# Kernel optimization log

Hardware: AMD Instinct MI355X
Metric: run time of the kernel (lower is better)

Reference implementation:

```python
import jax, jax.numpy as jnp
import numpy as np


def setup_inputs() -> dict:
    key = jax.random.key(0)
    k1, k2 = jax.random.split(key)
    B, N, M, D = 32, 1024, 1024, 256
    h1 = jax.random.normal(k1, (B, N, D), dtype=jnp.float32)
    h2 = jax.random.normal(k2, (B, M, D), dtype=jnp.float32)
    return {"h1": h1, "h2": h2}


def reference(h1, h2):
    # Soft Hausdorff over B graph pairs.
    # torch cdist with p=2 here is sum_d |x-y|^2 == squared L2 distance;
    N = h1.shape[1]
    M = h2.shape[1]
    sq1 = jnp.sum(h1 * h1, axis=-1)  # [B, N]
    sq2 = jnp.sum(h2 * h2, axis=-1)  # [B, M]
    cross = jnp.einsum('bnd,bmd->bnm', h1, h2)  # [B, N, M]
    dist = sq1[:, :, None] + sq2[:, None, :] - 2.0 * cross
    dist = jnp.maximum(dist, 0.0)  # guard tiny negative fp noise
    a = jnp.min(dist, axis=1).sum(axis=-1)  # min over N for each col, then sum over M
    b = jnp.min(dist, axis=2).sum(axis=-1)  # min over M for each row, then sum over N
    return (a + b) / min(N, M)  # [B]
```

## Files before the change

kernel.cpp:

```cpp
#include <hip/hip_runtime.h>
#include <hip/hip_bf16.h>
#include <stdint.h>

#define BB 32
#define NN 1024
#define MM 1024
#define DD 256

typedef __attribute__((ext_vector_type(8))) short short8;
typedef __attribute__((ext_vector_type(4))) float floatx4;

__device__ inline unsigned short f2bf(float x) {
    union { __hip_bfloat16 h; unsigned short u; } cv;
    cv.h = __float2bfloat16(x);
    return cv.u;
}

__device__ inline void async_copy16(void* lds, const void* g) {
    __builtin_amdgcn_global_load_lds(
        (const __attribute__((address_space(1))) unsigned int*)g,
        (__attribute__((address_space(3))) unsigned int*)lds, 16, 0, 0);
}
__device__ inline void async_copy4(void* lds, const void* g) {
    __builtin_amdgcn_global_load_lds(
        (const __attribute__((address_space(1))) unsigned int*)g,
        (__attribute__((address_space(3))) unsigned int*)lds, 4, 0, 0);
}

__global__ __launch_bounds__(256) void convert_kernel(
        const float* __restrict__ h1, const float* __restrict__ h2,
        unsigned short* __restrict__ h1b, unsigned short* __restrict__ h2b,
        float* __restrict__ sq1, float* __restrict__ sq2,
        unsigned int* __restrict__ minb) {
    int g = blockIdx.x * 256 + threadIdx.x;
    if (g < 2 * BB * NN) minb[g] = 0x7F800000u;

    int wid  = blockIdx.x * 4 + (threadIdx.x >> 6);
    int lane = threadIdx.x & 63;
    int l5   = lane & 31;
    int row  = wid * 2 + (lane >> 5);
    const int total1 = BB * NN;

    const float* src; unsigned short* dst; float* sq; int r;
    if (row < total1) { src = h1; dst = h1b; sq = sq1; r = row; }
    else              { src = h2; dst = h2b; sq = sq2; r = row - total1; }

    const float4* p = (const float4*)(src + (size_t)r * DD) + l5 * 2;
    float4 a = p[0], c = p[1];

    float s = a.x*a.x + a.y*a.y + a.z*a.z + a.w*a.w
            + c.x*c.x + c.y*c.y + c.z*c.z + c.w*c.w;
    #pragma unroll
    for (int off = 16; off; off >>= 1) s += __shfl_xor(s, off, 64);

    short8 o;
    o[0] = f2bf(a.x); o[1] = f2bf(a.y); o[2] = f2bf(a.z); o[3] = f2bf(a.w);
    o[4] = f2bf(c.x); o[5] = f2bf(c.y); o[6] = f2bf(c.z); o[7] = f2bf(c.w);
    *(short8*)((char*)(dst + (size_t)r * DD) + l5 * 16) = o;

    if (l5 == 0) sq[r] = s;
}

__global__ __launch_bounds__(512, 2) void gemm_kernel(
        const unsigned short* __restrict__ h1b, const unsigned short* __restrict__ h2b,
        const float* __restrict__ sq1, const float* __restrict__ sq2,
        unsigned int* __restrict__ rowmin, unsigned int* __restrict__ colmin) {
    __shared__ __align__(16) char pool[106496];
    #define BUF0 (pool + 65536)
    #define BUF1 (pool + 81920)
    #define BUF2 (pool + 0)
    #define BUF3 (pool + 16384)
    float*        sq2_lds = (float*)(pool + 98304);
    unsigned int* cl      = (unsigned int*)(pool + 102400);

    const int b    = blockIdx.x;
    const int tile = blockIdx.y;
    const int n0   = tile * 128;

    const int tid  = threadIdx.x;
    const int wave = tid >> 6;
    const int lane = tid & 63;
    const int wn   = (wave >> 2) * 64;
    const int wm   = (wave & 3) * 32;

    const char* Ag = (const char*)(h1b + ((size_t)b * NN + n0) * DD);
    const char* Bg = (const char*)(h2b + (size_t)b * MM * DD);

    const int krow = lane >> 4;
    const int rrow = lane & 15;
    const int rx   = rrow & 7;
    const int lrow = krow * 4;
    const int lcol = rrow;

    cl[tid] = 0x7F800000u; cl[tid + 512] = 0x7F800000u;

    const float4* s1p = (const float4*)(sq1 + b * NN + n0 + wn + lrow);
    float4 s1v4[4];
    #pragma unroll
    for (int i = 0; i < 4; ++i) s1v4[i] = s1p[i * 4];

    #pragma unroll
    for (int t = 0; t < 2; ++t)
        async_copy4(pool + 98304 + t * 2048 + wave * 256,
                    (const char*)(sq2 + b * MM) + t * 2048 + wave * 256 + lane * 4);

    #pragma unroll
    for (int t = 0; t < 8; ++t) {
        int ch = t * 8 + wave;
        int r  = ch * 2 + (lane >> 5);
        int cu = (lane & 31) ^ (r & 7);
        async_copy16(pool + ch * 1024, Ag + (size_t)r * 512 + (cu << 4));
    }

    const int rl  = lane >> 3;
    const int bcu = (lane & 7) ^ rl;
    #define STAGE(mt_, ks_, BUFP)                                             \
        {                                                                     \
            _Pragma("unroll")                                                 \
            for (int c = 0; c < 2; ++c) {                                     \
                int ch_ = wave * 2 + c;                                       \
                int r_  = ch_ * 8 + rl;                                       \
                async_copy16((char*)(BUFP) + ch_ * 1024,                      \
                             Bg + (size_t)((mt_) * 128 + r_) * 512            \
                                + (size_t)(ks_) * 128 + (bcu << 4));          \
            }                                                                 \
        }

    STAGE(0, 0, BUF0);
    STAGE(0, 1, BUF1);

    asm volatile("s_waitcnt vmcnt(4)" ::: "memory");
    __builtin_amdgcn_s_barrier();
    __builtin_amdgcn_sched_barrier(0);

    short8 af[4][8];
    #pragma unroll
    for (int i = 0; i < 4; ++i) {
        #pragma unroll
        for (int kq = 0; kq < 8; ++kq) {
            int u = (kq * 4 + krow) ^ rx;
            af[i][kq] = *(const short8*)(pool
                        + (size_t)(wn + i * 16 + rrow) * 512 + (u << 4));
        }
    }
    asm volatile("s_waitcnt lgkmcnt(0)" ::: "memory");
    __builtin_amdgcn_s_barrier();
    __builtin_amdgcn_sched_barrier(0);
    STAGE(0, 2, BUF2);

    float rmin[4][4];
    #pragma unroll
    for (int i = 0; i < 4; ++i)
        #pragma unroll
        for (int r = 0; r < 4; ++r) rmin[i][r] = 3.0e38f;

    #pragma unroll 1
    for (int mt = 0; mt < 8; ++mt) {
        floatx4 acc[4][2] = {};

        #pragma unroll
        for (int ks = 0; ks < 4; ++ks) {
            if (mt == 7 && ks == 2)      { asm volatile("s_waitcnt vmcnt(2)" ::: "memory"); }
            else if (mt == 7 && ks == 3) { asm volatile("s_waitcnt vmcnt(0)" ::: "memory"); }
            else                         { asm volatile("s_waitcnt vmcnt(4)" ::: "memory"); }
            __builtin_amdgcn_s_barrier();
            __builtin_amdgcn_sched_barrier(0);

            if (ks == 0)          { STAGE(mt,     3, BUF3); }
            else if (mt < 7) {
                if (ks == 1)      { STAGE(mt + 1, 0, BUF0); }
                else if (ks == 2) { STAGE(mt + 1, 1, BUF1); }
                else              { STAGE(mt + 1, 2, BUF2); }
            }

            const char* Bb = (ks == 0) ? BUF0 : (ks == 1) ? BUF1
                           : (ks == 2) ? BUF2 : BUF3;
            __builtin_amdgcn_s_setprio(1);
            #pragma unroll
            for (int kk = 0; kk < 2; ++kk) {
                const int u = ((kk << 2) | krow) ^ rx;
                short8 bfv[2];
                #pragma unroll
                for (int j = 0; j < 2; ++j)
                    bfv[j] = *(const short8*)(Bb
                             + (size_t)(wm + j * 16 + rrow) * 128 + (u << 4));
                #pragma unroll
                for (int i = 0; i < 4; ++i)
                    #pragma unroll
                    for (int j = 0; j < 2; ++j)
                        acc[i][j] = __builtin_amdgcn_mfma_f32_16x16x32_bf16(
                            af[i][ks * 2 + kk], bfv[j], acc[i][j], 0, 0, 0);
            }
            __builtin_amdgcn_s_setprio(0);
        }

        float s2v0 = sq2_lds[mt * 128 + wm + lcol];
        float s2v1 = sq2_lds[mt * 128 + wm + 16 + lcol];

        float cmin0 = 3.0e38f, cmin1 = 3.0e38f;
        #pragma unroll
        for (int i = 0; i < 4; ++i) {
            #pragma unroll
            for (int r = 0; r < 4; ++r) {
                float s1x = ((const float*)&s1v4[i])[r];
                float d0 = fmaxf(s1x + s2v0 - 2.0f * acc[i][0][r], 0.0f);
                float d1 = fmaxf(s1x + s2v1 - 2.0f * acc[i][1][r], 0.0f);
                rmin[i][r] = fminf(rmin[i][r], fminf(d0, d1));
                cmin0 = fminf(cmin0, d0);
                cmin1 = fminf(cmin1, d1);
            }
        }
        cmin0 = fminf(cmin0, __shfl_xor(cmin0, 16, 64));
        cmin0 = fminf(cmin0, __shfl_xor(cmin0, 32, 64));
        cmin1 = fminf(cmin1, __shfl_xor(cmin1, 16, 64));
        cmin1 = fminf(cmin1, __shfl_xor(cmin1, 32, 64));
        if (lane < 16) {
            atomicMin(&cl[mt * 128 + wm + lcol],      __float_as_uint(cmin0));
            atomicMin(&cl[mt * 128 + wm + 16 + lcol], __float_as_uint(cmin1));
        }
    }

    unsigned int* rm = rowmin + b * NN + n0;
    #pragma unroll
    for (int i = 0; i < 4; ++i) {
        #pragma unroll
        for (int r = 0; r < 4; ++r) {
            float v = rmin[i][r];
            #pragma unroll
            for (int off = 1; off < 16; off <<= 1)
                v = fminf(v, __shfl_xor(v, off, 64));
            if (lcol == 0)
                atomicMin(&rm[wn + i * 16 + lrow + r], __float_as_uint(v));
        }
    }

    __syncthreads();
    unsigned int* cmg = colmin + b * MM;
    atomicMin(&cmg[tid],       cl[tid]);
    atomicMin(&cmg[tid + 512], cl[tid + 512]);
    #undef STAGE
    #undef BUF0
    #undef BUF1
    #undef BUF2
    #undef BUF3
}

__global__ __launch_bounds__(256) void finalize_kernel(
        const unsigned int* __restrict__ rowmin,
        const unsigned int* __restrict__ colmin,
        float* __restrict__ out) {
    int b = blockIdx.x;
    int tid = threadIdx.x;
    float s = 0.0f;
    for (int i = tid; i < NN; i += 256) s += __uint_as_float(rowmin[b * NN + i]);
    for (int i = tid; i < MM; i += 256) s += __uint_as_float(colmin[b * MM + i]);
    #pragma unroll
    for (int off = 32; off; off >>= 1) s += __shfl_xor(s, off, 64);
    __shared__ float wsum[4];
    if ((tid & 63) == 0) wsum[tid >> 6] = s;
    __syncthreads();
    if (tid == 0) out[b] = (wsum[0] + wsum[1] + wsum[2] + wsum[3]) * (1.0f / 1024.0f);
}

extern "C" void kernel_launch(void* const* d_in, const int* in_sizes, int n_in,
                              void* d_out, int out_size, void* d_ws, size_t ws_size,
                              hipStream_t stream) {
    const float* h1 = (const float*)d_in[0];
    const float* h2 = (const float*)d_in[1];
    float* out = (float*)d_out;

    char* ws = (char*)d_ws;
    const size_t bf_bytes = (size_t)BB * NN * DD * sizeof(unsigned short);
    unsigned short* h1b = (unsigned short*)ws;
    unsigned short* h2b = (unsigned short*)(ws + bf_bytes);
    float* sq1 = (float*)(ws + 2 * bf_bytes);
    float* sq2 = sq1 + BB * NN;
    unsigned int* rowmin = (unsigned int*)(sq2 + BB * MM);
    unsigned int* colmin = rowmin + BB * NN;

    hipLaunchKernelGGL(convert_kernel, dim3(8192), dim3(256), 0, stream,
                       h1, h2, h1b, h2b, sq1, sq2, rowmin);

    hipLaunchKernelGGL(gemm_kernel, dim3(BB, 8), dim3(512), 0, stream,
                       h1b, h2b, sq1, sq2, rowmin, colmin);

    hipLaunchKernelGGL(finalize_kernel, dim3(BB), dim3(256), 0, stream,
                       rowmin, colmin, out);
}
```

Measured before the change: 47.42 us.

## Fuse fp32-to-bf16 conversion and norms into GEMM, drop convert kernel

Removes the separate conversion kernel. The GEMM kernel now stages fp32 tiles of h1 and h2 directly into LDS, converts them to bf16 in registers before the MFMAs, and computes the squared norms on the fly. This avoids writing and re-reading a bf16 copy of both inputs and saves a kernel launch. In exchange, B tiles are twice as large in LDS (about 136KB, limiting residency to one block per CU), and every block repeats the conversion and norm VALU work for h2. Global atomics are replaced by per-tile column partials and direct row-min stores, with the min over tiles moved into the finalize kernel.

```diff
diff --git a/kernel.cpp b/kernel.cpp
--- a/kernel.cpp
+++ b/kernel.cpp
@@ -15,63 +15,25 @@
     cv.h = __float2bfloat16(x);
     return cv.u;
 }
-
+__device__ inline short8 pack8(float4 a, float4 b) {
+    short8 o;
+    o[0] = f2bf(a.x); o[1] = f2bf(a.y); o[2] = f2bf(a.z); o[3] = f2bf(a.w);
+    o[4] = f2bf(b.x); o[5] = f2bf(b.y); o[6] = f2bf(b.z); o[7] = f2bf(b.w);
+    return o;
+}
 __device__ inline void async_copy16(void* lds, const void* g) {
     __builtin_amdgcn_global_load_lds(
         (const __attribute__((address_space(1))) unsigned int*)g,
         (__attribute__((address_space(3))) unsigned int*)lds, 16, 0, 0);
 }
-__device__ inline void async_copy4(void* lds, const void* g) {
-    __builtin_amdgcn_global_load_lds(
-        (const __attribute__((address_space(1))) unsigned int*)g,
-        (__attribute__((address_space(3))) unsigned int*)lds, 4, 0, 0);
-}
-
-__global__ __launch_bounds__(256) void convert_kernel(
+
+__global__ __launch_bounds__(512, 2) void gemm_kernel(
         const float* __restrict__ h1, const float* __restrict__ h2,
-        unsigned short* __restrict__ h1b, unsigned short* __restrict__ h2b,
-        float* __restrict__ sq1, float* __restrict__ sq2,
-        unsigned int* __restrict__ minb) {
-    int g = blockIdx.x * 256 + threadIdx.x;
-    if (g < 2 * BB * NN) minb[g] = 0x7F800000u;
-
-    int wid  = blockIdx.x * 4 + (threadIdx.x >> 6);
-    int lane = threadIdx.x & 63;
-    int l5   = lane & 31;
-    int row  = wid * 2 + (lane >> 5);
-    const int total1 = BB * NN;
-
-    const float* src; unsigned short* dst; float* sq; int r;
-    if (row < total1) { src = h1; dst = h1b; sq = sq1; r = row; }
-    else              { src = h2; dst = h2b; sq = sq2; r = row - total1; }
-
-    const float4* p = (const float4*)(src + (size_t)r * DD) + l5 * 2;
-    float4 a = p[0], c = p[1];
-
-    float s = a.x*a.x + a.y*a.y + a.z*a.z + a.w*a.w
-            + c.x*c.x + c.y*c.y + c.z*c.z + c.w*c.w;
-    #pragma unroll
-    for (int off = 16; off; off >>= 1) s += __shfl_xor(s, off, 64);
-
-    short8 o;
-    o[0] = f2bf(a.x); o[1] = f2bf(a.y); o[2] = f2bf(a.z); o[3] = f2bf(a.w);
-    o[4] = f2bf(c.x); o[5] = f2bf(c.y); o[6] = f2bf(c.z); o[7] = f2bf(c.w);
-    *(short8*)((char*)(dst + (size_t)r * DD) + l5 * 16) = o;
-
-    if (l5 == 0) sq[r] = s;
-}
-
-__global__ __launch_bounds__(512, 2) void gemm_kernel(
-        const unsigned short* __restrict__ h1b, const unsigned short* __restrict__ h2b,
-        const float* __restrict__ sq1, const float* __restrict__ sq2,
-        unsigned int* __restrict__ rowmin, unsigned int* __restrict__ colmin) {
-    __shared__ __align__(16) char pool[106496];
-    #define BUF0 (pool + 65536)
-    #define BUF1 (pool + 81920)
-    #define BUF2 (pool + 0)
-    #define BUF3 (pool + 16384)
-    float*        sq2_lds = (float*)(pool + 98304);
-    unsigned int* cl      = (unsigned int*)(pool + 102400);
+        unsigned int* __restrict__ rowmin, unsigned int* __restrict__ colpart) {
+    __shared__ __align__(16) char pool[136192];
+    float*        sq1_lds = (float*)(pool + 131072);
+    unsigned int* cl      = (unsigned int*)(pool + 131584);
+    unsigned int* rlds    = (unsigned int*)(pool + 135680);
 
     const int b    = blockIdx.x;
     const int tile = blockIdx.y;
@@ -83,76 +45,79 @@
     const int wn   = (wave >> 2) * 64;
     const int wm   = (wave & 3) * 32;
 
-    const char* Ag = (const char*)(h1b + ((size_t)b * NN + n0) * DD);
-    const char* Bg = (const char*)(h2b + (size_t)b * MM * DD);
-
     const int krow = lane >> 4;
     const int rrow = lane & 15;
     const int rx   = rrow & 7;
     const int lrow = krow * 4;
     const int lcol = rrow;
 
+    const char* Ag = (const char*)(h1 + ((size_t)b * NN + n0) * DD);
+    const char* Bg = (const char*)(h2 + (size_t)b * MM * DD);
+
     cl[tid] = 0x7F800000u; cl[tid + 512] = 0x7F800000u;
-
-    const float4* s1p = (const float4*)(sq1 + b * NN + n0 + wn + lrow);
-    float4 s1v4[4];
-    #pragma unroll
-    for (int i = 0; i < 4; ++i) s1v4[i] = s1p[i * 4];
-
-    #pragma unroll
-    for (int t = 0; t < 2; ++t)
-        async_copy4(pool + 98304 + t * 2048 + wave * 256,
-                    (const char*)(sq2 + b * MM) + t * 2048 + wave * 256 + lane * 4);
-
-    #pragma unroll
-    for (int t = 0; t < 8; ++t) {
-        int ch = t * 8 + wave;
-        int r  = ch * 2 + (lane >> 5);
-        int cu = (lane & 31) ^ (r & 7);
-        async_copy16(pool + ch * 1024, Ag + (size_t)r * 512 + (cu << 4));
-    }
-
-    const int rl  = lane >> 3;
-    const int bcu = (lane & 7) ^ rl;
-    #define STAGE(mt_, ks_, BUFP)                                             \
-        {                                                                     \
-            _Pragma("unroll")                                                 \
-            for (int c = 0; c < 2; ++c) {                                     \
-                int ch_ = wave * 2 + c;                                       \
-                int r_  = ch_ * 8 + rl;                                       \
-                async_copy16((char*)(BUFP) + ch_ * 1024,                      \
-                             Bg + (size_t)((mt_) * 128 + r_) * 512            \
-                                + (size_t)(ks_) * 128 + (bcu << 4));          \
-            }                                                                 \
-        }
-
-    STAGE(0, 0, BUF0);
-    STAGE(0, 1, BUF1);
-
-    asm volatile("s_waitcnt vmcnt(4)" ::: "memory");
+    if (tid < 128) rlds[tid] = 0x7F800000u;
+
+    #pragma unroll
+    for (int t = 0; t < 16; ++t) {
+        int r = t * 8 + wave;
+        async_copy16(pool + r * 1024,
+                     Ag + (size_t)r * 1024 + ((lane ^ ((r & 7) << 1)) << 4));
+    }
+    asm volatile("s_waitcnt vmcnt(0) lgkmcnt(0)" ::: "memory");
     __builtin_amdgcn_s_barrier();
     __builtin_amdgcn_sched_barrier(0);
 
     short8 af[4][8];
-    #pragma unroll
-    for (int i = 0; i < 4; ++i) {
-        #pragma unroll
-        for (int kq = 0; kq < 8; ++kq) {
-            int u = (kq * 4 + krow) ^ rx;
-            af[i][kq] = *(const short8*)(pool
-                        + (size_t)(wn + i * 16 + rrow) * 512 + (u << 4));
+    {
+        float ssum[4] = {0.f, 0.f, 0.f, 0.f};
+        #pragma unroll
+        for (int i = 0; i < 4; ++i) {
+            const char* rp = pool + (size_t)(wn + i * 16 + rrow) * 1024;
+            #pragma unroll
+            for (int kq = 0; kq < 8; ++kq) {
+                int u0 = ((kq << 3) + (krow << 1)) ^ (rx << 1);
+                float4 f0 = *(const float4*)(rp + (u0 << 4));
+                float4 f1 = *(const float4*)(rp + ((u0 | 1) << 4));
+                af[i][kq] = pack8(f0, f1);
+                if ((wave & 3) == 0)
+                    ssum[i] += f0.x*f0.x + f0.y*f0.y + f0.z*f0.z + f0.w*f0.w
+                             + f1.x*f1.x + f1.y*f1.y + f1.z*f1.z + f1.w*f1.w;
+            }
+        }
+        if ((wave & 3) == 0) {
+            #pragma unroll
+            for (int i = 0; i < 4; ++i) {
+                float s = ssum[i];
+                s += __shfl_xor(s, 16, 64);
+                s += __shfl_xor(s, 32, 64);
+                if (lane < 16) sq1_lds[wn + i * 16 + rrow] = s;
+            }
         }
     }
     asm volatile("s_waitcnt lgkmcnt(0)" ::: "memory");
+    __builtin_amdgcn_sched_barrier(0);
     __builtin_amdgcn_s_barrier();
     __builtin_amdgcn_sched_barrier(0);
-    STAGE(0, 2, BUF2);
+
+    const int rl4 = lane >> 4;
+    const int pu  = lane & 15;
+    #define STAGE(mt_, ks_, boff_)                                            \
+        { _Pragma("unroll")                                                   \
+          for (int c = 0; c < 4; ++c) {                                       \
+            int ch_ = wave * 4 + c;                                           \
+            int r_  = ch_ * 4 + rl4;                                          \
+            async_copy16(pool + (boff_) + ch_ * 1024,                         \
+                Bg + (size_t)((mt_) * 128 + r_) * 1024 + (size_t)(ks_) * 256  \
+                   + ((pu ^ ((r_ & 7) << 1)) << 4)); } }
+
+    STAGE(0, 0, 0); STAGE(0, 1, 32768); STAGE(0, 2, 65536);
 
     float rmin[4][4];
     #pragma unroll
     for (int i = 0; i < 4; ++i)
         #pragma unroll
         for (int r = 0; r < 4; ++r) rmin[i][r] = 3.0e38f;
+    float s2a0 = 0.f, s2a1 = 0.f;
 
     #pragma unroll 1
     for (int mt = 0; mt < 8; ++mt) {
@@ -160,51 +125,57 @@
 
         #pragma unroll
         for (int ks = 0; ks < 4; ++ks) {
-            if (mt == 7 && ks == 2)      { asm volatile("s_waitcnt vmcnt(2)" ::: "memory"); }
+            if (mt == 7 && ks == 2)      { asm volatile("s_waitcnt vmcnt(4)" ::: "memory"); }
             else if (mt == 7 && ks == 3) { asm volatile("s_waitcnt vmcnt(0)" ::: "memory"); }
-            else                         { asm volatile("s_waitcnt vmcnt(4)" ::: "memory"); }
+            else                         { asm volatile("s_waitcnt vmcnt(8)" ::: "memory"); }
             __builtin_amdgcn_s_barrier();
             __builtin_amdgcn_sched_barrier(0);
 
-            if (ks == 0)          { STAGE(mt,     3, BUF3); }
+            if (ks == 0)          { STAGE(mt,     3, 98304); }
             else if (mt < 7) {
-                if (ks == 1)      { STAGE(mt + 1, 0, BUF0); }
-                else if (ks == 2) { STAGE(mt + 1, 1, BUF1); }
-                else              { STAGE(mt + 1, 2, BUF2); }
-            }
-
-            const char* Bb = (ks == 0) ? BUF0 : (ks == 1) ? BUF1
-                           : (ks == 2) ? BUF2 : BUF3;
+                if (ks == 1)      { STAGE(mt + 1, 0, 0);     }
+                else if (ks == 2) { STAGE(mt + 1, 1, 32768); }
+                else              { STAGE(mt + 1, 2, 65536); }
+            }
+
+            const char* Bb = pool + ((ks == 0) ? 0 : (ks == 1) ? 32768
+                                   : (ks == 2) ? 65536 : 98304);
             __builtin_amdgcn_s_setprio(1);
             #pragma unroll
             for (int kk = 0; kk < 2; ++kk) {
-                const int u = ((kk << 2) | krow) ^ rx;
-                short8 bfv[2];
                 #pragma unroll
-                for (int j = 0; j < 2; ++j)
-                    bfv[j] = *(const short8*)(Bb
-                             + (size_t)(wm + j * 16 + rrow) * 128 + (u << 4));
-                #pragma unroll
-                for (int i = 0; i < 4; ++i)
+                for (int j = 0; j < 2; ++j) {
+                    const char* rp = Bb + (size_t)(wm + j * 16 + rrow) * 256;
+                    int v0 = (((kk << 2) + krow) << 1) ^ (rx << 1);
+                    float4 g0 = *(const float4*)(rp + (v0 << 4));
+                    float4 g1 = *(const float4*)(rp + ((v0 | 1) << 4));
+                    short8 bv = pack8(g0, g1);
                     #pragma unroll
-                    for (int j = 0; j < 2; ++j)
+                    for (int i = 0; i < 4; ++i)
                         acc[i][j] = __builtin_amdgcn_mfma_f32_16x16x32_bf16(
-                            af[i][ks * 2 + kk], bfv[j], acc[i][j], 0, 0, 0);
+                            af[i][ks * 2 + kk], bv, acc[i][j], 0, 0, 0);
+                    float d = g0.x*g0.x + g0.y*g0.y + g0.z*g0.z + g0.w*g0.w
+                            + g1.x*g1.x + g1.y*g1.y + g1.z*g1.z + g1.w*g1.w;
+                    if (j == 0) s2a0 += d; else s2a1 += d;
+                }
             }
             __builtin_amdgcn_s_setprio(0);
         }
 
-        float s2v0 = sq2_lds[mt * 128 + wm + lcol];
-        float s2v1 = sq2_lds[mt * 128 + wm + 16 + lcol];
+        float s20 = s2a0; s20 += __shfl_xor(s20, 16, 64); s20 += __shfl_xor(s20, 32, 64);
+        float s21 = s2a1; s21 += __shfl_xor(s21, 16, 64); s21 += __shfl_xor(s21, 32, 64);
+        s2a0 = 0.f; s2a1 = 0.f;
 
         float cmin0 = 3.0e38f, cmin1 = 3.0e38f;
         #pragma unroll
         for (int i = 0; i < 4; ++i) {
+            float4 s1q = *(const float4*)((const char*)sq1_lds
+                        + ((wn + i * 16 + lrow) << 2));
             #pragma unroll
             for (int r = 0; r < 4; ++r) {
-                float s1x = ((const float*)&s1v4[i])[r];
-                float d0 = fmaxf(s1x + s2v0 - 2.0f * acc[i][0][r], 0.0f);
-                float d1 = fmaxf(s1x + s2v1 - 2.0f * acc[i][1][r], 0.0f);
+                float s1x = ((const float*)&s1q)[r];
+                float d0 = fmaxf(s1x + s20 - 2.0f * acc[i][0][r], 0.0f);
+                float d1 = fmaxf(s1x + s21 - 2.0f * acc[i][1][r], 0.0f);
                 rmin[i][r] = fminf(rmin[i][r], fminf(d0, d1));
                 cmin0 = fminf(cmin0, d0);
                 cmin1 = fminf(cmin1, d1);
@@ -220,7 +191,6 @@
         }
     }
 
-    unsigned int* rm = rowmin + b * NN + n0;
     #pragma unroll
     for (int i = 0; i < 4; ++i) {
         #pragma unroll
@@ -230,30 +200,35 @@
             for (int off = 1; off < 16; off <<= 1)
                 v = fminf(v, __shfl_xor(v, off, 64));
             if (lcol == 0)
-                atomicMin(&rm[wn + i * 16 + lrow + r], __float_as_uint(v));
-        }
-    }
-
+                atomicMin(&rlds[wn + i * 16 + lrow + r], __float_as_uint(v));
+        }
+    }
     __syncthreads();
-    unsigned int* cmg = colmin + b * MM;
-    atomicMin(&cmg[tid],       cl[tid]);
-    atomicMin(&cmg[tid + 512], cl[tid + 512]);
+
+    unsigned int* cp = colpart + ((size_t)b * 8 + tile) * 1024;
+    cp[tid]       = cl[tid];
+    cp[tid + 512] = cl[tid + 512];
+    if (tid < 128) rowmin[b * NN + n0 + tid] = rlds[tid];
     #undef STAGE
-    #undef BUF0
-    #undef BUF1
-    #undef BUF2
-    #undef BUF3
 }
 
 __global__ __launch_bounds__(256) void finalize_kernel(
         const unsigned int* __restrict__ rowmin,
-        const unsigned int* __restrict__ colmin,
+        const unsigned int* __restrict__ colpart,
         float* __restrict__ out) {
     int b = blockIdx.x;
     int tid = threadIdx.x;
     float s = 0.0f;
-    for (int i = tid; i < NN; i += 256) s += __uint_as_float(rowmin[b * NN + i]);
-    for (int i = tid; i < MM; i += 256) s += __uint_as_float(colmin[b * MM + i]);
+    #pragma unroll
+    for (int t = 0; t < 4; ++t) {
+        int m = tid + t * 256;
+        s += __uint_as_float(rowmin[b * NN + m]);
+        unsigned int v = colpart[(size_t)b * 8192 + m];
+        #pragma unroll
+        for (int q = 1; q < 8; ++q)
+            v = min(v, colpart[(size_t)b * 8192 + q * 1024 + m]);
+        s += __uint_as_float(v);
+    }
     #pragma unroll
     for (int off = 32; off; off >>= 1) s += __shfl_xor(s, off, 64);
     __shared__ float wsum[4];
@@ -269,21 +244,12 @@
     const float* h2 = (const float*)d_in[1];
     float* out = (float*)d_out;
 
-    char* ws = (char*)d_ws;
-    const size_t bf_bytes = (size_t)BB * NN * DD * sizeof(unsigned short);
-    unsigned short* h1b = (unsigned short*)ws;
-    unsigned short* h2b = (unsigned short*)(ws + bf_bytes);
-    float* sq1 = (float*)(ws + 2 * bf_bytes);
-    float* sq2 = sq1 + BB * NN;
-    unsigned int* rowmin = (unsigned int*)(sq2 + BB * MM);
-    unsigned int* colmin = rowmin + BB * NN;
-
-    hipLaunchKernelGGL(convert_kernel, dim3(8192), dim3(256), 0, stream,
-                       h1, h2, h1b, h2b, sq1, sq2, rowmin);
+    unsigned int* rowmin  = (unsigned int*)d_ws;
+    unsigned int* colpart = rowmin + BB * NN;
 
     hipLaunchKernelGGL(gemm_kernel, dim3(BB, 8), dim3(512), 0, stream,
-                       h1b, h2b, sq1, sq2, rowmin, colmin);
+                       h1, h2, rowmin, colpart);
 
     hipLaunchKernelGGL(finalize_kernel, dim3(BB), dim3(256), 0, stream,
-                       rowmin, colmin, out);
-}
+                       rowmin, colpart, out);
+}
```

Measured after the change: 131.4 us. 2.77x slower.

## Fuse h1 bf16 conversion and norm computation into the GEMM kernel

Applied to the files above, without the earlier changes.

The convert kernel now processes only h2. The GEMM kernel loads its fp32 h1 tile directly into LDS in two halves, converts it to bf16 register fragments and computes the row squared norms in place. This removes the global write and re-read of a bf16 copy of h1 and halves the convert pass. The cost is that the GEMM prologue becomes serialized and heavier, with twice the fp32 bytes loaded, extra waits and barriers, and sq1 is now read from LDS in the epilogue.

```diff
diff --git a/kernel.cpp b/kernel.cpp
--- a/kernel.cpp
+++ b/kernel.cpp
@@ -15,7 +15,12 @@
     cv.h = __float2bfloat16(x);
     return cv.u;
 }
-
+__device__ inline short8 pack8(float4 a, float4 b) {
+    short8 o;
+    o[0] = f2bf(a.x); o[1] = f2bf(a.y); o[2] = f2bf(a.z); o[3] = f2bf(a.w);
+    o[4] = f2bf(b.x); o[5] = f2bf(b.y); o[6] = f2bf(b.z); o[7] = f2bf(b.w);
+    return o;
+}
 __device__ inline void async_copy16(void* lds, const void* g) {
     __builtin_amdgcn_global_load_lds(
         (const __attribute__((address_space(1))) unsigned int*)g,
@@ -28,10 +33,8 @@
 }
 
 __global__ __launch_bounds__(256) void convert_kernel(
-        const float* __restrict__ h1, const float* __restrict__ h2,
-        unsigned short* __restrict__ h1b, unsigned short* __restrict__ h2b,
-        float* __restrict__ sq1, float* __restrict__ sq2,
-        unsigned int* __restrict__ minb) {
+        const float* __restrict__ h2, unsigned short* __restrict__ h2b,
+        float* __restrict__ sq2, unsigned int* __restrict__ minb) {
     int g = blockIdx.x * 256 + threadIdx.x;
     if (g < 2 * BB * NN) minb[g] = 0x7F800000u;
 
@@ -39,13 +42,8 @@
     int lane = threadIdx.x & 63;
     int l5   = lane & 31;
     int row  = wid * 2 + (lane >> 5);
-    const int total1 = BB * NN;
-
-    const float* src; unsigned short* dst; float* sq; int r;
-    if (row < total1) { src = h1; dst = h1b; sq = sq1; r = row; }
-    else              { src = h2; dst = h2b; sq = sq2; r = row - total1; }
-
-    const float4* p = (const float4*)(src + (size_t)r * DD) + l5 * 2;
+
+    const float4* p = (const float4*)(h2 + (size_t)row * DD) + l5 * 2;
     float4 a = p[0], c = p[1];
 
     float s = a.x*a.x + a.y*a.y + a.z*a.z + a.w*a.w
@@ -53,25 +51,22 @@
     #pragma unroll
     for (int off = 16; off; off >>= 1) s += __shfl_xor(s, off, 64);
 
-    short8 o;
-    o[0] = f2bf(a.x); o[1] = f2bf(a.y); o[2] = f2bf(a.z); o[3] = f2bf(a.w);
-    o[4] = f2bf(c.x); o[5] = f2bf(c.y); o[6] = f2bf(c.z); o[7] = f2bf(c.w);
-    *(short8*)((char*)(dst + (size_t)r * DD) + l5 * 16) = o;
-
-    if (l5 == 0) sq[r] = s;
+    *(short8*)((char*)(h2b + (size_t)row * DD) + l5 * 16) = pack8(a, c);
+    if (l5 == 0) sq2[row] = s;
 }
 
 __global__ __launch_bounds__(512, 2) void gemm_kernel(
-        const unsigned short* __restrict__ h1b, const unsigned short* __restrict__ h2b,
-        const float* __restrict__ sq1, const float* __restrict__ sq2,
+        const float* __restrict__ h1, const unsigned short* __restrict__ h2b,
+        const float* __restrict__ sq2,
         unsigned int* __restrict__ rowmin, unsigned int* __restrict__ colmin) {
-    __shared__ __align__(16) char pool[106496];
+    __shared__ __align__(16) char pool[98304];
     #define BUF0 (pool + 65536)
     #define BUF1 (pool + 81920)
     #define BUF2 (pool + 0)
     #define BUF3 (pool + 16384)
-    float*        sq2_lds = (float*)(pool + 98304);
-    unsigned int* cl      = (unsigned int*)(pool + 102400);
+    __shared__ __align__(16) float  sq1_s[128];
+    __shared__ __align__(16) float  sq2_s[1024];
+    __shared__ unsigned int cl_s[1024];
 
     const int b    = blockIdx.x;
     const int tile = blockIdx.y;
@@ -83,7 +78,7 @@
     const int wn   = (wave >> 2) * 64;
     const int wm   = (wave & 3) * 32;
 
-    const char* Ag = (const char*)(h1b + ((size_t)b * NN + n0) * DD);
+    const char* Ag = (const char*)(h1 + ((size_t)b * NN + n0) * DD);
     const char* Bg = (const char*)(h2b + (size_t)b * MM * DD);
 
     const int krow = lane >> 4;
@@ -92,24 +87,57 @@
     const int lrow = krow * 4;
     const int lcol = rrow;
 
-    cl[tid] = 0x7F800000u; cl[tid + 512] = 0x7F800000u;
-
-    const float4* s1p = (const float4*)(sq1 + b * NN + n0 + wn + lrow);
-    float4 s1v4[4];
-    #pragma unroll
-    for (int i = 0; i < 4; ++i) s1v4[i] = s1p[i * 4];
+    cl_s[tid] = 0x7F800000u; cl_s[tid + 512] = 0x7F800000u;
 
     #pragma unroll
     for (int t = 0; t < 2; ++t)
-        async_copy4(pool + 98304 + t * 2048 + wave * 256,
+        async_copy4((char*)sq2_s + t * 2048 + wave * 256,
                     (const char*)(sq2 + b * MM) + t * 2048 + wave * 256 + lane * 4);
 
-    #pragma unroll
-    for (int t = 0; t < 8; ++t) {
-        int ch = t * 8 + wave;
-        int r  = ch * 2 + (lane >> 5);
-        int cu = (lane & 31) ^ (r & 7);
-        async_copy16(pool + ch * 1024, Ag + (size_t)r * 512 + (cu << 4));
+    short8 af[4][8];
+
+    #pragma unroll 1
+    for (int half = 0; half < 2; ++half) {
+        #pragma unroll
+        for (int t = 0; t < 8; ++t) {
+            int r = t * 8 + wave;
+            async_copy16(pool + r * 1024,
+                         Ag + (size_t)(half * 64 + r) * 1024 + ((lane ^ (r & 7)) << 4));
+        }
+        asm volatile("s_waitcnt vmcnt(0) lgkmcnt(0)" ::: "memory");
+        __builtin_amdgcn_s_barrier();
+        __builtin_amdgcn_sched_barrier(0);
+
+        if ((wave >> 2) == half) {
+            float ssum[4] = {0.f, 0.f, 0.f, 0.f};
+            #pragma unroll
+            for (int i = 0; i < 4; ++i) {
+                const char* rp = pool + (size_t)(i * 16 + rrow) * 1024;
+                #pragma unroll
+                for (int kq = 0; kq < 8; ++kq) {
+                    int u0 = kq * 8 + krow * 2;
+                    float4 f0 = *(const float4*)(rp + ((u0 ^ rx) << 4));
+                    float4 f1 = *(const float4*)(rp + (((u0 + 1) ^ rx) << 4));
+                    af[i][kq] = pack8(f0, f1);
+                    if ((wave & 3) == 0)
+                        ssum[i] += f0.x*f0.x + f0.y*f0.y + f0.z*f0.z + f0.w*f0.w
+                                 + f1.x*f1.x + f1.y*f1.y + f1.z*f1.z + f1.w*f1.w;
+                }
+            }
+            if ((wave & 3) == 0) {
+                #pragma unroll
+                for (int i = 0; i < 4; ++i) {
+                    float s = ssum[i];
+                    s += __shfl_xor(s, 16, 64);
+                    s += __shfl_xor(s, 32, 64);
+                    if (lane < 16) sq1_s[wn + i * 16 + rrow] = s;
+                }
+            }
+        }
+        asm volatile("s_waitcnt lgkmcnt(0)" ::: "memory");
+        __builtin_amdgcn_sched_barrier(0);
+        __builtin_amdgcn_s_barrier();
+        __builtin_amdgcn_sched_barrier(0);
     }
 
     const int rl  = lane >> 3;
@@ -128,24 +156,6 @@
 
     STAGE(0, 0, BUF0);
     STAGE(0, 1, BUF1);
-
-    asm volatile("s_waitcnt vmcnt(4)" ::: "memory");
-    __builtin_amdgcn_s_barrier();
-    __builtin_amdgcn_sched_barrier(0);
-
-    short8 af[4][8];
-    #pragma unroll
-    for (int i = 0; i < 4; ++i) {
-        #pragma unroll
-        for (int kq = 0; kq < 8; ++kq) {
-            int u = (kq * 4 + krow) ^ rx;
-            af[i][kq] = *(const short8*)(pool
-                        + (size_t)(wn + i * 16 + rrow) * 512 + (u << 4));
-        }
-    }
-    asm volatile("s_waitcnt lgkmcnt(0)" ::: "memory");
-    __builtin_amdgcn_s_barrier();
-    __builtin_amdgcn_sched_barrier(0);
     STAGE(0, 2, BUF2);
 
     float rmin[4][4];
@@ -194,15 +204,16 @@
             __builtin_amdgcn_s_setprio(0);
         }
 
-        float s2v0 = sq2_lds[mt * 128 + wm + lcol];
-        float s2v1 = sq2_lds[mt * 128 + wm + 16 + lcol];
+        float s2v0 = sq2_s[mt * 128 + wm + lcol];
+        float s2v1 = sq2_s[mt * 128 + wm + 16 + lcol];
 
         float cmin0 = 3.0e38f, cmin1 = 3.0e38f;
         #pragma unroll
         for (int i = 0; i < 4; ++i) {
+            float4 s1q = *(const float4*)(&sq1_s[wn + i * 16 + lrow]);
             #pragma unroll
             for (int r = 0; r < 4; ++r) {
-                float s1x = ((const float*)&s1v4[i])[r];
+                float s1x = ((const float*)&s1q)[r];
                 float d0 = fmaxf(s1x + s2v0 - 2.0f * acc[i][0][r], 0.0f);
                 float d1 = fmaxf(s1x + s2v1 - 2.0f * acc[i][1][r], 0.0f);
                 rmin[i][r] = fminf(rmin[i][r], fminf(d0, d1));
@@ -215,8 +226,8 @@
         cmin1 = fminf(cmin1, __shfl_xor(cmin1, 16, 64));
         cmin1 = fminf(cmin1, __shfl_xor(cmin1, 32, 64));
         if (lane < 16) {
-            atomicMin(&cl[mt * 128 + wm + lcol],      __float_as_uint(cmin0));
-            atomicMin(&cl[mt * 128 + wm + 16 + lcol], __float_as_uint(cmin1));
+            atomicMin(&cl_s[mt * 128 + wm + lcol],      __float_as_uint(cmin0));
+            atomicMin(&cl_s[mt * 128 + wm + 16 + lcol], __float_as_uint(cmin1));
         }
     }
 
@@ -236,8 +247,8 @@
 
     __syncthreads();
     unsigned int* cmg = colmin + b * MM;
-    atomicMin(&cmg[tid],       cl[tid]);
-    atomicMin(&cmg[tid + 512], cl[tid + 512]);
+    atomicMin(&cmg[tid],       cl_s[tid]);
+    atomicMin(&cmg[tid + 512], cl_s[tid + 512]);
     #undef STAGE
     #undef BUF0
     #undef BUF1
@@ -270,19 +281,16 @@
     float* out = (float*)d_out;
 
     char* ws = (char*)d_ws;
-    const size_t bf_bytes = (size_t)BB * NN * DD * sizeof(unsigned short);
-    unsigned short* h1b = (unsigned short*)ws;
-    unsigned short* h2b = (unsigned short*)(ws + bf_bytes);
-    float* sq1 = (float*)(ws + 2 * bf_bytes);
-    float* sq2 = sq1 + BB * NN;
+    unsigned short* h2b = (unsigned short*)ws;
+    float* sq2          = (float*)(ws + (size_t)BB * MM * DD * 2);
     unsigned int* rowmin = (unsigned int*)(sq2 + BB * MM);
     unsigned int* colmin = rowmin + BB * NN;
 
-    hipLaunchKernelGGL(convert_kernel, dim3(8192), dim3(256), 0, stream,
-                       h1, h2, h1b, h2b, sq1, sq2, rowmin);
+    hipLaunchKernelGGL(convert_kernel, dim3(4096), dim3(256), 0, stream,
+                       h2, h2b, sq2, rowmin);
 
     hipLaunchKernelGGL(gemm_kernel, dim3(BB, 8), dim3(512), 0, stream,
-                       h1b, h2b, sq1, sq2, rowmin, colmin);
+                       h1, h2b, sq2, rowmin, colmin);
 
     hipLaunchKernelGGL(finalize_kernel, dim3(BB), dim3(256), 0, stream,
                        rowmin, colmin, out);
```

Result: slower. 68.07 us (+43.5%).
